# Kernel optimization log

Hardware: AMD Instinct MI355X
Metric: run time of the kernel (lower is better)

## Reference

```python
import jax, jax.numpy as jnp
import numpy as np

N_QUBITS = 8   # out_channels = number of wires
KERNEL = 4     # kernel_size
N_LAYERS = 4
STRIDE = 1
PAD = 1


def _rx(t):
    c = jnp.cos(t * 0.5).astype(jnp.complex64)
    s = jnp.sin(t * 0.5).astype(jnp.complex64)
    return jnp.stack([jnp.stack([c, -1j * s]), jnp.stack([-1j * s, c])])


def _ry(t):
    c = jnp.cos(t * 0.5).astype(jnp.complex64)
    s = jnp.sin(t * 0.5).astype(jnp.complex64)
    return jnp.stack([jnp.stack([c, -s]), jnp.stack([s, c])])


def _rz(t):
    e = jnp.exp(-0.5j * t.astype(jnp.complex64))
    z = jnp.zeros((), jnp.complex64)
    return jnp.stack([jnp.stack([e, z]), jnp.stack([z, jnp.conj(e)])])


def _ap1(state, U, w):
    # apply 2x2 gate U on qubit axis w of state shaped (2,)*N_QUBITS
    s = jnp.moveaxis(state, w, -1)
    s = s @ U.T
    return jnp.moveaxis(s, -1, w)


def _cnot(state, c, t):
    s0 = jax.lax.index_in_dim(state, 0, axis=c, keepdims=True)
    s1 = jax.lax.index_in_dim(state, 1, axis=c, keepdims=True)
    return jnp.concatenate([s0, jnp.flip(s1, axis=t)], axis=c)


def _ansatz(state, wl):  # wl: (N_QUBITS, 3) angles for layer i (custom_layers)
    for j in range(N_QUBITS):
        c, t = (j, j + 1) if j < N_QUBITS - 1 else (0, j)
        state = _ap1(state, _rx(wl[j, 0]), j)
        state = _cnot(state, c, t)
        state = _ap1(state, _ry(wl[j, 1]), j)
        state = _cnot(state, c, t)
        state = _ap1(state, _rz(wl[j, 2]), j)
    return state


def _circuit(inputs, weights):
    # inputs: (KERNEL,) patch; weights: (N_LAYERS+1, N_QUBITS, 3)
    state = jnp.zeros((2,) * N_QUBITS, jnp.complex64).at[(0,) * N_QUBITS].set(1.0)
    state = _ansatz(state, weights[0])
    for i in range(1, N_LAYERS + 1):
        w = 0
        for _ in range(N_QUBITS // KERNEL):  # 'parallel': re-upload data each layer
            for k in range(KERNEL):
                state = _ap1(state, _ry(inputs[k]), w + k)
            w += KERNEL
        state = _ansatz(state, weights[i])
    probs = state.real ** 2 + state.imag ** 2
    sign = jnp.array([1.0, -1.0], jnp.float32)
    z = [jnp.sum(probs, axis=tuple(a for a in range(N_QUBITS) if a != j)) @ sign
         for j in range(N_QUBITS)]
    return jnp.stack(z)  # (N_QUBITS,) <PauliZ_j>


def _forward(vector, weights):
    bs, ch, l = vector.shape
    if ch > 1:
        vector = vector.mean(axis=-2).reshape(bs, 1, l)
    v = jnp.pad(vector, ((0, 0), (0, 0), (PAD, PAD)))
    l_out = (l + 2 * PAD - KERNEL) // STRIDE + 1
    idx = jnp.arange(l_out)[:, None] * STRIDE + jnp.arange(KERNEL)  # (l_out, K)
    patches = v[:, 0, :][:, idx].reshape(bs * l_out, KERNEL)
    q = jax.vmap(_circuit, in_axes=(0, None))(patches, weights)  # (bs*l_out, N_QUBITS)
    out = q.reshape(bs, l_out, N_QUBITS).transpose(0, 2, 1)  # (bs, C, l_out)
    out = jax.nn.relu(out)
    return jnp.max(out, axis=-1, keepdims=True)  # (bs, C, 1)


def setup_inputs() -> dict:
    key = jax.random.key(0)
    k1, k2 = jax.random.split(key)
    vector = jax.random.normal(k1, (8, 1, 512), jnp.float32)
    # flax nn.initializers.normal() default stddev = 0.01
    weights = jax.random.normal(k2, (N_LAYERS + 1, N_QUBITS, 3), jnp.float32) * 0.01
    return {"vector": vector, "weights": weights}


def reference(vector, weights):
    return _forward(vector, weights)
```

## Files before the change

### kernel.cpp

```cpp
#include <hip/hip_runtime.h>

#define NQ 8
#define KK 4
#define NLAYERS 4
#define LIN 512
#define LOUT 511
#define BATCH 8
#define NCIRC (BATCH * LOUT)

__device__ float g_tab[240];
__device__ float g_st0[512];

template<int M> __device__ __forceinline__ float lx(float v) {
    if constexpr (M == 1)
        return __builtin_bit_cast(float, __builtin_amdgcn_update_dpp(
            0, __builtin_bit_cast(int, v), 0xB1, 0xF, 0xF, true));
    else if constexpr (M == 2)
        return __builtin_bit_cast(float, __builtin_amdgcn_update_dpp(
            0, __builtin_bit_cast(int, v), 0x4E, 0xF, 0xF, true));
    else if constexpr (M == 3)
        return __builtin_bit_cast(float, __builtin_amdgcn_update_dpp(
            0, __builtin_bit_cast(int, v), 0x1B, 0xF, 0xF, true));
    else if constexpr (M < 32)
        return __builtin_bit_cast(float, __builtin_amdgcn_ds_swizzle(
            __builtin_bit_cast(int, v), (M << 10) | 0x1F));
    else
        return __shfl_xor(v, M, 64);
}


template<int BP>
__device__ __forceinline__ void g_rx(float (&sr)[4], float (&si)[4], float c, float s, int lane) {
    if constexpr (BP >= 2) {
        constexpr int M = 1 << (BP - 2);
        #pragma unroll
        for (int r = 0; r < 4; ++r) {
            float orr = lx<M>(sr[r]);
            float oii = lx<M>(si[r]);
            float nr = c * sr[r] + s * oii;
            float ni = c * si[r] - s * orr;
            sr[r] = nr; si[r] = ni;
        }
    } else if constexpr (BP == 1) {
        #pragma unroll
        for (int p = 0; p < 2; ++p) {
            const int a = p, b = p + 2;
            float ar = sr[a], ai = si[a], br = sr[b], bi = si[b];
            sr[a] = c*ar + s*bi;  si[a] = c*ai - s*br;
            sr[b] = c*br + s*ai;  si[b] = c*bi - s*ar;
        }
    } else {
        #pragma unroll
        for (int p = 0; p < 2; ++p) {
            const int a = 2*p, b = 2*p + 1;
            float ar = sr[a], ai = si[a], br = sr[b], bi = si[b];
            sr[a] = c*ar + s*bi;  si[a] = c*ai - s*br;
            sr[b] = c*br + s*ai;  si[b] = c*bi - s*ar;
        }
    }
}

template<int BP>
__device__ __forceinline__ void g_ry(float (&sr)[4], float (&si)[4], float c, float s, int lane) {
    if constexpr (BP >= 2) {
        constexpr int M = 1 << (BP - 2);
        const float sg = ((lane >> (BP - 2)) & 1) ? s : -s;
        #pragma unroll
        for (int r = 0; r < 4; ++r) {
            float orr = lx<M>(sr[r]);
            float oii = lx<M>(si[r]);
            sr[r] = c * sr[r] + sg * orr;
            si[r] = c * si[r] + sg * oii;
        }
    } else if constexpr (BP == 1) {
        #pragma unroll
        for (int p = 0; p < 2; ++p) {
            const int a = p, b = p + 2;
            float ar = sr[a], ai = si[a], br = sr[b], bi = si[b];
            sr[a] = c*ar - s*br; si[a] = c*ai - s*bi;
            sr[b] = s*ar + c*br; si[b] = s*ai + c*bi;
        }
    } else {
        #pragma unroll
        for (int p = 0; p < 2; ++p) {
            const int a = 2*p, b = 2*p + 1;
            float ar = sr[a], ai = si[a], br = sr[b], bi = si[b];
            sr[a] = c*ar - s*br; si[a] = c*ai - s*bi;
            sr[b] = s*ar + c*br; si[b] = s*ai + c*bi;
        }
    }
}

template<int BP>
__device__ __forceinline__ void g_rz(float (&sr)[4], float (&si)[4], float c, float s, int lane) {
    if constexpr (BP >= 2) {
        const float t = ((lane >> (BP - 2)) & 1) ? -s : s;
        #pragma unroll
        for (int r = 0; r < 4; ++r) {
            float nr = c * sr[r] + t * si[r];
            float ni = c * si[r] - t * sr[r];
            sr[r] = nr; si[r] = ni;
        }
    } else if constexpr (BP == 1) {
        #pragma unroll
        for (int r = 0; r < 4; ++r) {
            const float t = (r < 2) ? s : -s;
            float nr = c * sr[r] + t * si[r];
            float ni = c * si[r] - t * sr[r];
            sr[r] = nr; si[r] = ni;
        }
    } else {
        #pragma unroll
        for (int r = 0; r < 4; ++r) {
            const float t = ((r & 1) == 0) ? s : -s;
            float nr = c * sr[r] + t * si[r];
            float ni = c * si[r] - t * sr[r];
            sr[r] = nr; si[r] = ni;
        }
    }
}

template<int BPC, int BPT>
__device__ __forceinline__ void g_fry(float (&sr)[4], float (&si)[4], float c, float s, int lane) {
    if constexpr (BPT >= 2) {
        constexpr int M = (1 << (BPC - 2)) | (1 << (BPT - 2));
        const float sg = ((lane >> (BPC - 2)) & 1) ? s : -s;
        #pragma unroll
        for (int r = 0; r < 4; ++r) {
            float orr = lx<M>(sr[r]);
            float oii = lx<M>(si[r]);
            sr[r] = c * sr[r] + sg * orr;
            si[r] = c * si[r] + sg * oii;
        }
    } else if constexpr (BPT == 1) {
        constexpr int M = 1 << (BPC - 2);
        const float sg = ((lane >> (BPC - 2)) & 1) ? s : -s;
        float pr[4], pi[4];
        #pragma unroll
        for (int r = 0; r < 4; ++r) { pr[r] = lx<M>(sr[r ^ 2]); pi[r] = lx<M>(si[r ^ 2]); }
        #pragma unroll
        for (int r = 0; r < 4; ++r) { sr[r] = c*sr[r] + sg*pr[r]; si[r] = c*si[r] + sg*pi[r]; }
    } else if constexpr (BPC == 1) {
        float t0r = sr[0], t0i = si[0], t1r = sr[1], t1i = si[1];
        sr[0] = c*sr[0] - s*sr[3];  si[0] = c*si[0] - s*si[3];
        sr[1] = c*sr[1] - s*sr[2];  si[1] = c*si[1] - s*si[2];
        sr[2] = c*sr[2] + s*t1r;    si[2] = c*si[2] + s*t1i;
        sr[3] = c*sr[3] + s*t0r;    si[3] = c*si[3] + s*t0i;
    } else {
        constexpr int M = 1 << (BPC - 2);
        const float sg = ((lane >> (BPC - 2)) & 1) ? s : -s;
        float pr[4], pi[4];
        #pragma unroll
        for (int r = 0; r < 4; ++r) { pr[r] = lx<M>(sr[r ^ 1]); pi[r] = lx<M>(si[r ^ 1]); }
        #pragma unroll
        for (int r = 0; r < 4; ++r) { sr[r] = c*sr[r] + sg*pr[r]; si[r] = c*si[r] + sg*pi[r]; }
    }
}

template<int J, bool DROP_RZ>
__device__ __forceinline__ void astep(float (&sr)[4], float (&si)[4],
                                      const float* __restrict__ t48, int lane) {
    constexpr int CQ = (J < 7) ? J : 0;
    constexpr int TQ = (J < 7) ? (J + 1) : 7;
    constexpr int BP = 7 - J, BPC = 7 - CQ, BPT = 7 - TQ;
    g_rx<BP>(sr, si, t48[J*6 + 0], t48[J*6 + 1], lane);
    g_fry<BPC, BPT>(sr, si, t48[J*6 + 2], t48[J*6 + 3], lane);
    if constexpr (!DROP_RZ)
        g_rz<BP>(sr, si, t48[J*6 + 4], t48[J*6 + 5], lane);
}

template<bool LAST>
__device__ __forceinline__ void ansatz_t(float (&sr)[4], float (&si)[4],
                                         const float* __restrict__ t48, int lane) {
    astep<0, LAST>(sr, si, t48, lane);
    astep<1, LAST>(sr, si, t48, lane);
    astep<2, LAST>(sr, si, t48, lane);
    astep<3, LAST>(sr, si, t48, lane);
    astep<4, LAST>(sr, si, t48, lane);
    astep<5, LAST>(sr, si, t48, lane);
    astep<6, LAST>(sr, si, t48, lane);
    astep<7, LAST>(sr, si, t48, lane);
}

template<int J>
__device__ __forceinline__ void astep0(float (&sr)[4], float (&si)[4],
                                       const float* __restrict__ wl, int lane) {
    constexpr int CQ = (J < 7) ? J : 0;
    constexpr int TQ = (J < 7) ? (J + 1) : 7;
    constexpr int BP = 7 - J, BPC = 7 - CQ, BPT = 7 - TQ;
    float a, c, s;
    a = 0.5f * wl[J*3 + 0]; s = __sinf(a); c = __cosf(a);
    g_rx<BP>(sr, si, c, s, lane);
    a = 0.5f * wl[J*3 + 1]; s = __sinf(a); c = __cosf(a);
    g_fry<BPC, BPT>(sr, si, c, s, lane);
    a = 0.5f * wl[J*3 + 2]; s = __sinf(a); c = __cosf(a);
    g_rz<BP>(sr, si, c, s, lane);
}

__device__ __forceinline__ void reup(float (&sr)[4], float (&si)[4],
                                     const float (&xc)[4], const float (&xs)[4], int lane) {
    g_ry<7>(sr, si, xc[0], xs[0], lane);  g_ry<3>(sr, si, xc[0], xs[0], lane);
    g_ry<6>(sr, si, xc[1], xs[1], lane);  g_ry<2>(sr, si, xc[1], xs[1], lane);
    g_ry<5>(sr, si, xc[2], xs[2], lane);  g_ry<1>(sr, si, xc[2], xs[2], lane);
    g_ry<4>(sr, si, xc[3], xs[3], lane);  g_ry<0>(sr, si, xc[3], xs[3], lane);
}

template<int ST>
__device__ __forceinline__ void bstage(float (&z)[8], int lane) {
    constexpr int M = 1 << ST;
    #pragma unroll
    for (int q = 0; q < 8; ++q) {
        float o = lx<M>(z[q]);
        if (q < 6 && (5 - q) == ST)
            z[q] = ((lane >> ST) & 1) ? (o - z[q]) : (z[q] - o);
        else
            z[q] += o;
    }
}

__global__ __launch_bounds__(256) void prep_kernel(const float* __restrict__ wts,
                                                   float* __restrict__ out) {
    const int t = threadIdx.x;
    if (t >= 192) {
        const int o = t - 192;
        if (o < BATCH * NQ) out[o] = 0.0f;
    } else if (t >= 64) {
        const int o = t - 64;
        if (o < 120) {
            float a = 0.5f * wts[o];
            g_tab[2*o]     = __cosf(a);
            g_tab[2*o + 1] = __sinf(a);
        }
    } else {
        const int lane = t;
        float sr[4] = {0.f, 0.f, 0.f, 0.f};
        float si[4] = {0.f, 0.f, 0.f, 0.f};
        if (lane == 0) sr[0] = 1.0f;
        astep0<0>(sr, si, wts, lane); astep0<1>(sr, si, wts, lane);
        astep0<2>(sr, si, wts, lane); astep0<3>(sr, si, wts, lane);
        astep0<4>(sr, si, wts, lane); astep0<5>(sr, si, wts, lane);
        astep0<6>(sr, si, wts, lane); astep0<7>(sr, si, wts, lane);
        #pragma unroll
        for (int r = 0; r < 4; ++r) {
            g_st0[(lane*4 + r)*2]     = sr[r];
            g_st0[(lane*4 + r)*2 + 1] = si[r];
        }
    }
}

__global__ __launch_bounds__(256) void quanv_kernel(const float* __restrict__ vec,
                                                    float* __restrict__ out) {
    const int lane = threadIdx.x & 63;
    const int w = threadIdx.x >> 6;
    const int wave = __builtin_amdgcn_readfirstlane(blockIdx.x * 4 + w);
    const int b = wave / LOUT;
    const int pos = wave - b * LOUT;

    float xc[4], xs[4];
    #pragma unroll
    for (int k = 0; k < KK; ++k) {
        int idx = pos - 1 + k;
        int ic = idx < 0 ? 0 : (idx > LIN - 1 ? LIN - 1 : idx);
        float xv = vec[b * LIN + ic];
        xv = (idx == ic) ? xv : 0.0f;
        float a = 0.5f * xv;
        xs[k] = __sinf(a); xc[k] = __cosf(a);
    }

    float sr[4], si[4];
    {
        const float4* st4 = (const float4*)g_st0;
        float4 a0 = st4[lane * 2], a1 = st4[lane * 2 + 1];
        sr[0] = a0.x; si[0] = a0.y; sr[1] = a0.z; si[1] = a0.w;
        sr[2] = a1.x; si[2] = a1.y; sr[3] = a1.z; si[3] = a1.w;
    }

    reup(sr, si, xc, xs, lane);  ansatz_t<false>(sr, si, g_tab + 1*48, lane);
    reup(sr, si, xc, xs, lane);  ansatz_t<false>(sr, si, g_tab + 2*48, lane);
    reup(sr, si, xc, xs, lane);  ansatz_t<false>(sr, si, g_tab + 3*48, lane);
    reup(sr, si, xc, xs, lane);  ansatz_t<true >(sr, si, g_tab + 4*48, lane);

    const float p0 = sr[0]*sr[0] + si[0]*si[0];
    const float p1 = sr[1]*sr[1] + si[1]*si[1];
    const float p2 = sr[2]*sr[2] + si[2]*si[2];
    const float p3 = sr[3]*sr[3] + si[3]*si[3];
    float z[8];
    const float pl = p0 + p1 + p2 + p3;
    #pragma unroll
    for (int q = 0; q < 6; ++q) z[q] = pl;
    z[6] = p0 + p1 - p2 - p3;
    z[7] = p0 - p1 + p2 - p3;

    bstage<0>(z, lane); bstage<1>(z, lane); bstage<2>(z, lane);
    bstage<3>(z, lane); bstage<4>(z, lane); bstage<5>(z, lane);

    __shared__ float zsh[4][NQ];
    __shared__ int bsh[4];
    if (lane == 0) {
        bsh[w] = b;
        #pragma unroll
        for (int q = 0; q < NQ; ++q) zsh[w][q] = fmaxf(z[q], 0.0f);
    }
    __syncthreads();
    if (lane < NQ) {
        const int q = lane;
        const bool leader = (w == 0) || (bsh[w] != bsh[w - 1]);
        if (leader) {
            float m = zsh[w][q];
            for (int w2 = w + 1; w2 < 4 && bsh[w2] == bsh[w]; ++w2)
                m = fmaxf(m, zsh[w2][q]);
            atomicMax((unsigned int*)(out + bsh[w] * NQ + q), __float_as_uint(m));
        }
    }
}

extern "C" void kernel_launch(void* const* d_in, const int* in_sizes, int n_in,
                              void* d_out, int out_size, void* d_ws, size_t ws_size,
                              hipStream_t stream) {
    const float* vec = (const float*)d_in[0];
    const float* wts = (const float*)d_in[1];
    float* out = (float*)d_out;

    hipLaunchKernelGGL(prep_kernel, dim3(1), dim3(256), 0, stream, wts, out);
    hipLaunchKernelGGL(quanv_kernel, dim3(NCIRC / 4), dim3(256), 0, stream, vec, out);
}
```

Measured before the change: 75.48 us.

## Map each circuit to 16 lanes with 16 amplitudes per lane

```diff
diff --git a/kernel.cpp b/kernel.cpp
--- a/kernel.cpp
+++ b/kernel.cpp
@@ -2,7 +2,6 @@
 
 #define NQ 8
 #define KK 4
-#define NLAYERS 4
 #define LIN 512
 #define LOUT 511
 #define BATCH 8
@@ -28,15 +27,13 @@
         return __shfl_xor(v, M, 64);
 }
 
-
 template<int BP>
-__device__ __forceinline__ void g_rx(float (&sr)[4], float (&si)[4], float c, float s, int lane) {
+__device__ __forceinline__ void g_rx4(float (&sr)[4], float (&si)[4], float c, float s, int lane) {
     if constexpr (BP >= 2) {
         constexpr int M = 1 << (BP - 2);
         #pragma unroll
         for (int r = 0; r < 4; ++r) {
-            float orr = lx<M>(sr[r]);
-            float oii = lx<M>(si[r]);
+            float orr = lx<M>(sr[r]), oii = lx<M>(si[r]);
             float nr = c * sr[r] + s * oii;
             float ni = c * si[r] - s * orr;
             sr[r] = nr; si[r] = ni;
@@ -61,38 +58,7 @@
 }
 
 template<int BP>
-__device__ __forceinline__ void g_ry(float (&sr)[4], float (&si)[4], float c, float s, int lane) {
-    if constexpr (BP >= 2) {
-        constexpr int M = 1 << (BP - 2);
-        const float sg = ((lane >> (BP - 2)) & 1) ? s : -s;
-        #pragma unroll
-        for (int r = 0; r < 4; ++r) {
-            float orr = lx<M>(sr[r]);
-            float oii = lx<M>(si[r]);
-            sr[r] = c * sr[r] + sg * orr;
-            si[r] = c * si[r] + sg * oii;
-        }
-    } else if constexpr (BP == 1) {
-        #pragma unroll
-        for (int p = 0; p < 2; ++p) {
-            const int a = p, b = p + 2;
-            float ar = sr[a], ai = si[a], br = sr[b], bi = si[b];
-            sr[a] = c*ar - s*br; si[a] = c*ai - s*bi;
-            sr[b] = s*ar + c*br; si[b] = s*ai + c*bi;
-        }
-    } else {
-        #pragma unroll
-        for (int p = 0; p < 2; ++p) {
-            const int a = 2*p, b = 2*p + 1;
-            float ar = sr[a], ai = si[a], br = sr[b], bi = si[b];
-            sr[a] = c*ar - s*br; si[a] = c*ai - s*bi;
-            sr[b] = s*ar + c*br; si[b] = s*ai + c*bi;
-        }
-    }
-}
-
-template<int BP>
-__device__ __forceinline__ void g_rz(float (&sr)[4], float (&si)[4], float c, float s, int lane) {
+__device__ __forceinline__ void g_rz4(float (&sr)[4], float (&si)[4], float c, float s, int lane) {
     if constexpr (BP >= 2) {
         const float t = ((lane >> (BP - 2)) & 1) ? -s : s;
         #pragma unroll
@@ -121,14 +87,13 @@
 }
 
 template<int BPC, int BPT>
-__device__ __forceinline__ void g_fry(float (&sr)[4], float (&si)[4], float c, float s, int lane) {
+__device__ __forceinline__ void g_fry4(float (&sr)[4], float (&si)[4], float c, float s, int lane) {
     if constexpr (BPT >= 2) {
         constexpr int M = (1 << (BPC - 2)) | (1 << (BPT - 2));
         const float sg = ((lane >> (BPC - 2)) & 1) ? s : -s;
         #pragma unroll
         for (int r = 0; r < 4; ++r) {
-            float orr = lx<M>(sr[r]);
-            float oii = lx<M>(si[r]);
+            float orr = lx<M>(sr[r]), oii = lx<M>(si[r]);
             sr[r] = c * sr[r] + sg * orr;
             si[r] = c * si[r] + sg * oii;
         }
@@ -157,62 +122,157 @@
     }
 }
 
-template<int J, bool DROP_RZ>
-__device__ __forceinline__ void astep(float (&sr)[4], float (&si)[4],
-                                      const float* __restrict__ t48, int lane) {
+template<int J>
+__device__ __forceinline__ void astep4(float (&sr)[4], float (&si)[4],
+                                       const float* __restrict__ t48, int lane) {
     constexpr int CQ = (J < 7) ? J : 0;
     constexpr int TQ = (J < 7) ? (J + 1) : 7;
     constexpr int BP = 7 - J, BPC = 7 - CQ, BPT = 7 - TQ;
-    g_rx<BP>(sr, si, t48[J*6 + 0], t48[J*6 + 1], lane);
-    g_fry<BPC, BPT>(sr, si, t48[J*6 + 2], t48[J*6 + 3], lane);
-    if constexpr (!DROP_RZ)
-        g_rz<BP>(sr, si, t48[J*6 + 4], t48[J*6 + 5], lane);
-}
-
-template<bool LAST>
-__device__ __forceinline__ void ansatz_t(float (&sr)[4], float (&si)[4],
-                                         const float* __restrict__ t48, int lane) {
-    astep<0, LAST>(sr, si, t48, lane);
-    astep<1, LAST>(sr, si, t48, lane);
-    astep<2, LAST>(sr, si, t48, lane);
-    astep<3, LAST>(sr, si, t48, lane);
-    astep<4, LAST>(sr, si, t48, lane);
-    astep<5, LAST>(sr, si, t48, lane);
-    astep<6, LAST>(sr, si, t48, lane);
-    astep<7, LAST>(sr, si, t48, lane);
-}
-
-template<int J>
-__device__ __forceinline__ void astep0(float (&sr)[4], float (&si)[4],
-                                       const float* __restrict__ wl, int lane) {
-    constexpr int CQ = (J < 7) ? J : 0;
-    constexpr int TQ = (J < 7) ? (J + 1) : 7;
-    constexpr int BP = 7 - J, BPC = 7 - CQ, BPT = 7 - TQ;
-    float a, c, s;
-    a = 0.5f * wl[J*3 + 0]; s = __sinf(a); c = __cosf(a);
-    g_rx<BP>(sr, si, c, s, lane);
-    a = 0.5f * wl[J*3 + 1]; s = __sinf(a); c = __cosf(a);
-    g_fry<BPC, BPT>(sr, si, c, s, lane);
-    a = 0.5f * wl[J*3 + 2]; s = __sinf(a); c = __cosf(a);
-    g_rz<BP>(sr, si, c, s, lane);
-}
-
-__device__ __forceinline__ void reup(float (&sr)[4], float (&si)[4],
-                                     const float (&xc)[4], const float (&xs)[4], int lane) {
-    g_ry<7>(sr, si, xc[0], xs[0], lane);  g_ry<3>(sr, si, xc[0], xs[0], lane);
-    g_ry<6>(sr, si, xc[1], xs[1], lane);  g_ry<2>(sr, si, xc[1], xs[1], lane);
-    g_ry<5>(sr, si, xc[2], xs[2], lane);  g_ry<1>(sr, si, xc[2], xs[2], lane);
-    g_ry<4>(sr, si, xc[3], xs[3], lane);  g_ry<0>(sr, si, xc[3], xs[3], lane);
+    g_rx4<BP>(sr, si, t48[J*6 + 0], t48[J*6 + 1], lane);
+    g_fry4<BPC, BPT>(sr, si, t48[J*6 + 2], t48[J*6 + 3], lane);
+    g_rz4<BP>(sr, si, t48[J*6 + 4], t48[J*6 + 5], lane);
+}
+
+template<int LB>
+__device__ __forceinline__ void rx_lane(float (&sr)[16], float (&si)[16], float c, float s) {
+    constexpr int M = 1 << LB;
+    #pragma unroll
+    for (int r = 0; r < 16; ++r) {
+        float orr = lx<M>(sr[r]), oii = lx<M>(si[r]);
+        float nr = c * sr[r] + s * oii;
+        float ni = c * si[r] - s * orr;
+        sr[r] = nr; si[r] = ni;
+    }
+}
+
+template<int LB>
+__device__ __forceinline__ void ry_lane(float (&sr)[16], float (&si)[16], float c, float s, int pos) {
+    constexpr int M = 1 << LB;
+    const float sg = ((pos >> LB) & 1) ? s : -s;
+    #pragma unroll
+    for (int r = 0; r < 16; ++r) {
+        float orr = lx<M>(sr[r]), oii = lx<M>(si[r]);
+        sr[r] = c * sr[r] + sg * orr;
+        si[r] = c * si[r] + sg * oii;
+    }
+}
+
+template<int LB>
+__device__ __forceinline__ void rz_lane(float (&sr)[16], float (&si)[16], float c, float s, int pos) {
+    const float t = ((pos >> LB) & 1) ? -s : s;
+    #pragma unroll
+    for (int r = 0; r < 16; ++r) {
+        float nr = c * sr[r] + t * si[r];
+        float ni = c * si[r] - t * sr[r];
+        sr[r] = nr; si[r] = ni;
+    }
+}
+
+template<int RB>
+__device__ __forceinline__ void rx_reg(float (&sr)[16], float (&si)[16], float c, float s) {
+    constexpr int m = 1 << RB;
+    #pragma unroll
+    for (int r = 0; r < 16; ++r) {
+        if ((r & m) == 0) {
+            const int a = r, b = r | m;
+            float ar = sr[a], ai = si[a], br = sr[b], bi = si[b];
+            sr[a] = c*ar + s*bi;  si[a] = c*ai - s*br;
+            sr[b] = c*br + s*ai;  si[b] = c*bi - s*ar;
+        }
+    }
+}
+
+template<int RB>
+__device__ __forceinline__ void ry_reg(float (&sr)[16], float (&si)[16], float c, float s) {
+    constexpr int m = 1 << RB;
+    #pragma unroll
+    for (int r = 0; r < 16; ++r) {
+        if ((r & m) == 0) {
+            const int a = r, b = r | m;
+            float ar = sr[a], ai = si[a], br = sr[b], bi = si[b];
+            sr[a] = c*ar - s*br;  si[a] = c*ai - s*bi;
+            sr[b] = s*ar + c*br;  si[b] = s*ai + c*bi;
+        }
+    }
+}
+
+template<int RB>
+__device__ __forceinline__ void rz_reg(float (&sr)[16], float (&si)[16], float c, float s) {
+    #pragma unroll
+    for (int r = 0; r < 16; ++r) {
+        const float t = ((r >> RB) & 1) ? -s : s;
+        float nr = c * sr[r] + t * si[r];
+        float ni = c * si[r] - t * sr[r];
+        sr[r] = nr; si[r] = ni;
+    }
+}
+
+template<int LBc, int LBt>
+__device__ __forceinline__ void fry_ll(float (&sr)[16], float (&si)[16], float c, float s, int pos) {
+    constexpr int M = (1 << LBc) | (1 << LBt);
+    const float sg = ((pos >> LBc) & 1) ? s : -s;
+    #pragma unroll
+    for (int r = 0; r < 16; ++r) {
+        float orr = lx<M>(sr[r]), oii = lx<M>(si[r]);
+        sr[r] = c * sr[r] + sg * orr;
+        si[r] = c * si[r] + sg * oii;
+    }
+}
+
+template<int LBc, int RBt>
+__device__ __forceinline__ void fry_lr(float (&sr)[16], float (&si)[16], float c, float s, int pos) {
+    constexpr int M = 1 << LBc;
+    constexpr int mt = 1 << RBt;
+    const float sg = ((pos >> LBc) & 1) ? s : -s;
+    float pr[16], pi[16];
+    #pragma unroll
+    for (int r = 0; r < 16; ++r) { pr[r] = lx<M>(sr[r ^ mt]); pi[r] = lx<M>(si[r ^ mt]); }
+    #pragma unroll
+    for (int r = 0; r < 16; ++r) { sr[r] = c*sr[r] + sg*pr[r]; si[r] = c*si[r] + sg*pi[r]; }
+}
+
+template<int RBc, int RBt>
+__device__ __forceinline__ void fry_rr(float (&sr)[16], float (&si)[16], float c, float s) {
+    constexpr int mm = (1 << RBc) | (1 << RBt);
+    float nr[16], ni[16];
+    #pragma unroll
+    for (int r = 0; r < 16; ++r) {
+        const float sg = ((r >> RBc) & 1) ? s : -s;
+        nr[r] = c*sr[r] + sg*sr[r ^ mm];
+        ni[r] = c*si[r] + sg*si[r ^ mm];
+    }
+    #pragma unroll
+    for (int r = 0; r < 16; ++r) { sr[r] = nr[r]; si[r] = ni[r]; }
+}
+
+__device__ __forceinline__ void ansatz16(float (&sr)[16], float (&si)[16],
+                                         const float* __restrict__ t, int pos) {
+    rx_lane<3>(sr, si, t[0], t[1]);   fry_ll<3,2>(sr, si, t[2], t[3], pos);   rz_lane<3>(sr, si, t[4], t[5], pos);
+    rx_lane<2>(sr, si, t[6], t[7]);   fry_ll<2,1>(sr, si, t[8], t[9], pos);   rz_lane<2>(sr, si, t[10], t[11], pos);
+    rx_lane<1>(sr, si, t[12], t[13]); fry_ll<1,0>(sr, si, t[14], t[15], pos); rz_lane<1>(sr, si, t[16], t[17], pos);
+    rx_lane<0>(sr, si, t[18], t[19]); fry_lr<0,3>(sr, si, t[20], t[21], pos); rz_lane<0>(sr, si, t[22], t[23], pos);
+    rx_reg<3>(sr, si, t[24], t[25]);  fry_rr<3,2>(sr, si, t[26], t[27]);      rz_reg<3>(sr, si, t[28], t[29]);
+    rx_reg<2>(sr, si, t[30], t[31]);  fry_rr<2,1>(sr, si, t[32], t[33]);      rz_reg<2>(sr, si, t[34], t[35]);
+    rx_reg<1>(sr, si, t[36], t[37]);  fry_rr<1,0>(sr, si, t[38], t[39]);      rz_reg<1>(sr, si, t[40], t[41]);
+    rx_reg<0>(sr, si, t[42], t[43]);  fry_lr<3,0>(sr, si, t[44], t[45], pos); rz_reg<0>(sr, si, t[46], t[47]);
+}
+
+__device__ __forceinline__ void reup16(float (&sr)[16], float (&si)[16],
+                                       const float (&xc)[4], const float (&xs)[4], int pos) {
+    ry_lane<3>(sr, si, xc[0], xs[0], pos);  ry_reg<3>(sr, si, xc[0], xs[0]);
+    ry_lane<2>(sr, si, xc[1], xs[1], pos);  ry_reg<2>(sr, si, xc[1], xs[1]);
+    ry_lane<1>(sr, si, xc[2], xs[2], pos);  ry_reg<1>(sr, si, xc[2], xs[2]);
+    ry_lane<0>(sr, si, xc[3], xs[3], pos);  ry_reg<0>(sr, si, xc[3], xs[3]);
 }
 
 template<int ST>
-__device__ __forceinline__ void bstage(float (&z)[8], int lane) {
+__device__ __forceinline__ void bstage16(float (&z)[8], int pos) {
     constexpr int M = 1 << ST;
     #pragma unroll
     for (int q = 0; q < 8; ++q) {
         float o = lx<M>(z[q]);
-        if (q < 6 && (5 - q) == ST)
-            z[q] = ((lane >> ST) & 1) ? (o - z[q]) : (z[q] - o);
+        if (q < 4 && (3 - q) == ST)
+            z[q] = ((pos >> ST) & 1) ? (o - z[q]) : (z[q] - o);
         else
             z[q] += o;
     }
@@ -220,26 +280,25 @@
 
 __global__ __launch_bounds__(256) void prep_kernel(const float* __restrict__ wts,
                                                    float* __restrict__ out) {
+    __shared__ float tt[240];
     const int t = threadIdx.x;
-    if (t >= 192) {
-        const int o = t - 192;
-        if (o < BATCH * NQ) out[o] = 0.0f;
-    } else if (t >= 64) {
-        const int o = t - 64;
-        if (o < 120) {
-            float a = 0.5f * wts[o];
-            g_tab[2*o]     = __cosf(a);
-            g_tab[2*o + 1] = __sinf(a);
-        }
-    } else {
+    if (t < 120) {
+        float a = 0.5f * wts[t];
+        float cv = __cosf(a), sv = __sinf(a);
+        g_tab[2*t] = cv;  g_tab[2*t + 1] = sv;
+        tt[2*t] = cv;     tt[2*t + 1] = sv;
+    }
+    if (t >= 192 && t < 192 + BATCH * NQ) out[t - 192] = 0.0f;
+    __syncthreads();
+    if (t < 64) {
         const int lane = t;
         float sr[4] = {0.f, 0.f, 0.f, 0.f};
         float si[4] = {0.f, 0.f, 0.f, 0.f};
         if (lane == 0) sr[0] = 1.0f;
-        astep0<0>(sr, si, wts, lane); astep0<1>(sr, si, wts, lane);
-        astep0<2>(sr, si, wts, lane); astep0<3>(sr, si, wts, lane);
-        astep0<4>(sr, si, wts, lane); astep0<5>(sr, si, wts, lane);
-        astep0<6>(sr, si, wts, lane); astep0<7>(sr, si, wts, lane);
+        astep4<0>(sr, si, tt, lane); astep4<1>(sr, si, tt, lane);
+        astep4<2>(sr, si, tt, lane); astep4<3>(sr, si, tt, lane);
+        astep4<4>(sr, si, tt, lane); astep4<5>(sr, si, tt, lane);
+        astep4<6>(sr, si, tt, lane); astep4<7>(sr, si, tt, lane);
         #pragma unroll
         for (int r = 0; r < 4; ++r) {
             g_st0[(lane*4 + r)*2]     = sr[r];
@@ -248,18 +307,19 @@
     }
 }
 
-__global__ __launch_bounds__(256) void quanv_kernel(const float* __restrict__ vec,
-                                                    float* __restrict__ out) {
-    const int lane = threadIdx.x & 63;
-    const int w = threadIdx.x >> 6;
-    const int wave = __builtin_amdgcn_readfirstlane(blockIdx.x * 4 + w);
-    const int b = wave / LOUT;
-    const int pos = wave - b * LOUT;
+__global__ __launch_bounds__(256, 1) void quanv_kernel(const float* __restrict__ vec,
+                                                       float* __restrict__ out) {
+    const int tid = threadIdx.x;
+    const int pos = tid & 15;
+    int circ = blockIdx.x * 16 + (tid >> 4);
+    if (circ > NCIRC - 1) circ = NCIRC - 1;
+    const int b = circ / LOUT;
+    const int op = circ - b * LOUT;
 
     float xc[4], xs[4];
     #pragma unroll
     for (int k = 0; k < KK; ++k) {
-        int idx = pos - 1 + k;
+        int idx = op - 1 + k;
         int ic = idx < 0 ? 0 : (idx > LIN - 1 ? LIN - 1 : idx);
         float xv = vec[b * LIN + ic];
         xv = (idx == ic) ? xv : 0.0f;
@@ -267,49 +327,58 @@
         xs[k] = __sinf(a); xc[k] = __cosf(a);
     }
 
-    float sr[4], si[4];
+    float sr[16], si[16];
     {
         const float4* st4 = (const float4*)g_st0;
-        float4 a0 = st4[lane * 2], a1 = st4[lane * 2 + 1];
-        sr[0] = a0.x; si[0] = a0.y; sr[1] = a0.z; si[1] = a0.w;
-        sr[2] = a1.x; si[2] = a1.y; sr[3] = a1.z; si[3] = a1.w;
-    }
-
-    reup(sr, si, xc, xs, lane);  ansatz_t<false>(sr, si, g_tab + 1*48, lane);
-    reup(sr, si, xc, xs, lane);  ansatz_t<false>(sr, si, g_tab + 2*48, lane);
-    reup(sr, si, xc, xs, lane);  ansatz_t<false>(sr, si, g_tab + 3*48, lane);
-    reup(sr, si, xc, xs, lane);  ansatz_t<true >(sr, si, g_tab + 4*48, lane);
-
-    const float p0 = sr[0]*sr[0] + si[0]*si[0];
-    const float p1 = sr[1]*sr[1] + si[1]*si[1];
-    const float p2 = sr[2]*sr[2] + si[2]*si[2];
-    const float p3 = sr[3]*sr[3] + si[3]*si[3];
+        #pragma unroll
+        for (int h = 0; h < 8; ++h) {
+            float4 v4 = st4[pos * 8 + h];
+            sr[2*h]   = v4.x; si[2*h]   = v4.y;
+            sr[2*h+1] = v4.z; si[2*h+1] = v4.w;
+        }
+    }
+
+    #pragma unroll 1
+    for (int L = 1; L <= 4; ++L) {
+        reup16(sr, si, xc, xs, pos);
+        ansatz16(sr, si, g_tab + L * 48, pos);
+    }
+
+    float p[16];
+    #pragma unroll
+    for (int r = 0; r < 16; ++r) p[r] = sr[r]*sr[r] + si[r]*si[r];
+    float pl = 0.f, z4 = 0.f, z5 = 0.f, z6 = 0.f, z7 = 0.f;
+    #pragma unroll
+    for (int r = 0; r < 16; ++r) {
+        pl += p[r];
+        z4 += ((r >> 3) & 1) ? -p[r] : p[r];
+        z5 += ((r >> 2) & 1) ? -p[r] : p[r];
+        z6 += ((r >> 1) & 1) ? -p[r] : p[r];
+        z7 += ( r       & 1) ? -p[r] : p[r];
+    }
     float z[8];
-    const float pl = p0 + p1 + p2 + p3;
-    #pragma unroll
-    for (int q = 0; q < 6; ++q) z[q] = pl;
-    z[6] = p0 + p1 - p2 - p3;
-    z[7] = p0 - p1 + p2 - p3;
-
-    bstage<0>(z, lane); bstage<1>(z, lane); bstage<2>(z, lane);
-    bstage<3>(z, lane); bstage<4>(z, lane); bstage<5>(z, lane);
-
-    __shared__ float zsh[4][NQ];
-    __shared__ int bsh[4];
-    if (lane == 0) {
-        bsh[w] = b;
-        #pragma unroll
-        for (int q = 0; q < NQ; ++q) zsh[w][q] = fmaxf(z[q], 0.0f);
+    z[0] = pl; z[1] = pl; z[2] = pl; z[3] = pl;
+    z[4] = z4; z[5] = z5; z[6] = z6; z[7] = z7;
+
+    bstage16<0>(z, pos); bstage16<1>(z, pos); bstage16<2>(z, pos); bstage16<3>(z, pos);
+
+    __shared__ float zsh[16][NQ];
+    __shared__ int bsh[16];
+    const int g = tid >> 4;
+    if (pos == 0) {
+        bsh[g] = b;
+        #pragma unroll
+        for (int q = 0; q < NQ; ++q) zsh[g][q] = fmaxf(z[q], 0.0f);
     }
     __syncthreads();
-    if (lane < NQ) {
-        const int q = lane;
-        const bool leader = (w == 0) || (bsh[w] != bsh[w - 1]);
+    if (tid < 128) {
+        const int gg = tid >> 3, q = tid & 7;
+        const bool leader = (gg == 0) || (bsh[gg] != bsh[gg - 1]);
         if (leader) {
-            float m = zsh[w][q];
-            for (int w2 = w + 1; w2 < 4 && bsh[w2] == bsh[w]; ++w2)
-                m = fmaxf(m, zsh[w2][q]);
-            atomicMax((unsigned int*)(out + bsh[w] * NQ + q), __float_as_uint(m));
+            float m = zsh[gg][q];
+            for (int g2 = gg + 1; g2 < 16 && bsh[g2] == bsh[gg]; ++g2)
+                m = fmaxf(m, zsh[g2][q]);
+            atomicMax((unsigned int*)(out + bsh[gg] * NQ + q), __float_as_uint(m));
         }
     }
 }
@@ -322,5 +391,6 @@
     float* out = (float*)d_out;
 
     hipLaunchKernelGGL(prep_kernel, dim3(1), dim3(256), 0, stream, wts, out);
-    hipLaunchKernelGGL(quanv_kernel, dim3(NCIRC / 4), dim3(256), 0, stream, vec, out);
-}
+    const int blocks = (NCIRC + 15) / 16;
+    hipLaunchKernelGGL(quanv_kernel, dim3(blocks), dim3(256), 0, stream, vec, out);
+}
```

After: 79.95 us. +5.9%, slower.
